# Kernel tuning notes

Measured on AMD Instinct MI355X. Metric: run time of the kernel, lower is better.

The kernel has to match this reference:

```python
import jax, jax.numpy as jnp
import numpy as np
import math

B, SQ, SK = 8, 1024, 1024
DIM_Q = DIM_K = DIM_V = 512
H = 8
EPS = 1e-5
INF = jnp.float32(1e38)


def _ln(x, g, b):
    mu = jnp.mean(x, axis=-1, keepdims=True)
    var = jnp.mean(jnp.square(x - mu), axis=-1, keepdims=True)
    return (x - mu) * jax.lax.rsqrt(var + EPS) * g + b


def setup_inputs() -> dict:
    key = jax.random.key(0)
    ks = jax.random.split(key, 12)
    s = 1.0 / math.sqrt(DIM_V)
    return {
        "queries": jax.random.normal(ks[0], (B, SQ, DIM_Q), jnp.float32),
        "keys": jax.random.normal(ks[1], (B, SK, DIM_K), jnp.float32),
        # binary presence masks (as in the original usage)
        "presence_q": (jax.random.uniform(ks[2], (B, SQ)) > 0.1).astype(jnp.float32),
        "presence_k": (jax.random.uniform(ks[3], (B, SK)) > 0.1).astype(jnp.float32),
        "num_heads": H,
        "Wq": jax.random.normal(ks[4], (DIM_Q, DIM_V), jnp.float32) * s,
        "bq": jnp.zeros((DIM_V,), jnp.float32),
        "Wk": jax.random.normal(ks[5], (DIM_K, DIM_V), jnp.float32) * s,
        "bk": jnp.zeros((DIM_V,), jnp.float32),
        "Wv": jax.random.normal(ks[6], (DIM_K, DIM_V), jnp.float32) * s,
        "bv": jnp.zeros((DIM_V,), jnp.float32),
        "Wo": jax.random.normal(ks[7], (DIM_V, DIM_V), jnp.float32) * s,
        "bo": jnp.zeros((DIM_V,), jnp.float32),
        "g0": jnp.ones((DIM_V,), jnp.float32),
        "b0": jnp.zeros((DIM_V,), jnp.float32),
        "g1": jnp.ones((DIM_V,), jnp.float32),
        "b1": jnp.zeros((DIM_V,), jnp.float32),
    }


def reference(queries, keys, presence_q, presence_k, num_heads,
              Wq, bq, Wk, bk, Wv, bv, Wo, bo, g0, b0, g1, b1):
    b, sq, _ = queries.shape
    dim_v = Wq.shape[1]
    d = dim_v // num_heads
    q = queries @ Wq + bq                              # [B,Sq,V]
    k = keys @ Wk + bk                                 # [B,Sk,V]
    v = keys @ Wv + bv                                 # [B,Sk,V]
    qh = q.reshape(b, sq, num_heads, d)
    kh = k.reshape(b, -1, num_heads, d)
    vh = v.reshape(b, -1, num_heads, d)
    logits = jnp.einsum('bqhd,bkhd->bhqk', qh, kh) / jnp.float32(math.sqrt(dim_v))
    pq = presence_q[:, None, :, None]                  # [B,1,Sq,1]
    logits = pq * logits - (1.0 - pq) * INF
    pk = presence_k[:, None, None, :]                  # [B,1,1,Sk]
    logits = pk * logits - (1.0 - pk) * INF
    A = jax.nn.softmax(logits, axis=-1)                # [B,H,Sq,Sk]
    o = qh + jnp.einsum('bhqk,bkhd->bqhd', A, vh)      # residual add of Q_
    o = o.reshape(b, sq, dim_v)
    o = _ln(o, g0, b0)
    o = o + jax.nn.relu(o @ Wo + bo)
    o = _ln(o, g1, b1)
    return o
```

## Files before the change

### kernel.cpp

```cpp
#include <hip/hip_runtime.h>

typedef __attribute__((ext_vector_type(8))) short short8;
typedef __attribute__((ext_vector_type(4))) float f32x4;

#define SCALE2 0.06375871571f

__device__ __forceinline__ float bfu(unsigned short u){
  return __uint_as_float(((unsigned int)u) << 16);
}
__device__ __forceinline__ unsigned short f2b(float x){
  unsigned int b = __float_as_uint(x);
  return (unsigned short)((b + 0x7fffu + ((b>>16)&1u)) >> 16);
}
__device__ __forceinline__ uint4 pack8(const float* f){
  float4 a = *(const float4*)f, b = *(const float4*)(f+4);
  uint4 r;
  r.x = (unsigned)f2b(a.x) | ((unsigned)f2b(a.y)<<16);
  r.y = (unsigned)f2b(a.z) | ((unsigned)f2b(a.w)<<16);
  r.z = (unsigned)f2b(b.x) | ((unsigned)f2b(b.y)<<16);
  r.w = (unsigned)f2b(b.z) | ((unsigned)f2b(b.w)<<16);
  return r;
}

__global__ __launch_bounds__(256) void prep_inputs(
    const float* Wq, const float* Wk, const float* Wv, const float* Wo,
    const float* q, const float* k, unsigned short* wt, unsigned short* qk_dst)
{
  const int id = blockIdx.x, t = threadIdx.x;
  if (id < 256){
    const int m = id >> 6;
    const float* W = (m==0)?Wq:(m==1)?Wk:(m==2)?Wv:Wo;
    unsigned short* dst = wt + (long)m*262144;
    __shared__ unsigned short tile[64][72];
    const int n0 = ((id>>3)&7)*64, k0 = (id&7)*64;
    {
      int r = t>>2, c0 = (t&3)*16;
      uint4 u0 = pack8(W + (long)(k0+r)*512 + n0 + c0);
      uint4 u1 = pack8(W + (long)(k0+r)*512 + n0 + c0 + 8);
      unsigned short* us0 = (unsigned short*)&u0;
      unsigned short* us1 = (unsigned short*)&u1;
      #pragma unroll
      for (int i=0;i<8;++i) tile[c0+i][r] = us0[i];
      #pragma unroll
      for (int i=0;i<8;++i) tile[c0+8+i][r] = us1[i];
    }
    __syncthreads();
    {
      int n = t>>2, ks = (t&3)*16;
      *(uint4*)(dst + (long)(n0+n)*512 + k0 + ks)     = *(uint4*)&tile[n][ks];
      *(uint4*)(dst + (long)(n0+n)*512 + k0 + ks + 8) = *(uint4*)&tile[n][ks+8];
    }
  } else {
    long i = ((long)(id-256)*256 + t)*8;
    const float* src = (i < 4194304) ? q + i : k + (i - 4194304);
    *(uint4*)(qk_dst + i) = pack8(src);
  }
}

__global__ __launch_bounds__(256) void proj_mfma(
    const unsigned short* qin, const unsigned short* kin, const unsigned short* wt,
    const float* bq, const float* bk, const float* bv,
    unsigned short* q_bf, unsigned short* k_bf, unsigned short* vt_bf)
{
  const int mat = blockIdx.z;
  const unsigned short* A = (mat==0)? qin : kin;
  const unsigned short* Wt = wt + (long)mat*262144;
  const float* bias = (mat==0)?bq:(mat==1)?bk:bv;
  const int row0 = blockIdx.y*128, col0 = blockIdx.x*128;
  __shared__ unsigned short As[2][128][40];
  __shared__ unsigned short Ws[2][128][40];
  const int t = threadIdx.x;
  const int lane = t & 63, wid = t >> 6;
  const int ln = lane & 15, quad = lane >> 4;
  const int wy = wid >> 1, wx = wid & 1;
  f32x4 acc[4][4];
  #pragma unroll
  for (int i=0;i<4;++i){
    #pragma unroll
    for (int j=0;j<4;++j) acc[i][j] = (f32x4){0.f,0.f,0.f,0.f};
  }
  const int sr = t>>1, sk0 = (t&1)*16;
  const unsigned short* Arow = A  + (long)(row0+sr)*512 + sk0;
  const unsigned short* Wrow = Wt + (long)(col0+sr)*512 + sk0;
  uint4 a0 = *(const uint4*)(Arow);
  uint4 a1 = *(const uint4*)(Arow + 8);
  uint4 w0 = *(const uint4*)(Wrow);
  uint4 w1 = *(const uint4*)(Wrow + 8);
  *(uint4*)&As[0][sr][sk0]   = a0;
  *(uint4*)&As[0][sr][sk0+8] = a1;
  *(uint4*)&Ws[0][sr][sk0]   = w0;
  *(uint4*)&Ws[0][sr][sk0+8] = w1;
  __syncthreads();
  for (int it=0; it<16; ++it){
    const int cur = it & 1;
    if (it < 15){
      a0 = *(const uint4*)(Arow + (it+1)*32);
      a1 = *(const uint4*)(Arow + (it+1)*32 + 8);
      w0 = *(const uint4*)(Wrow + (it+1)*32);
      w1 = *(const uint4*)(Wrow + (it+1)*32 + 8);
    }
    short8 a[4], b[4];
    #pragma unroll
    for (int mt=0;mt<4;++mt) a[mt] = *(const short8*)&As[cur][wy*64+mt*16+ln][quad*8];
    #pragma unroll
    for (int nt=0;nt<4;++nt) b[nt] = *(const short8*)&Ws[cur][wx*64+nt*16+ln][quad*8];
    #pragma unroll
    for (int mt=0;mt<4;++mt){
      #pragma unroll
      for (int nt=0;nt<4;++nt)
        acc[mt][nt] = __builtin_amdgcn_mfma_f32_16x16x32_bf16(a[mt], b[nt], acc[mt][nt], 0,0,0);
    }
    if (it < 15){
      *(uint4*)&As[cur^1][sr][sk0]   = a0;
      *(uint4*)&As[cur^1][sr][sk0+8] = a1;
      *(uint4*)&Ws[cur^1][sr][sk0]   = w0;
      *(uint4*)&Ws[cur^1][sr][sk0+8] = w1;
    }
    __syncthreads();
  }
  float bias_v[4];
  #pragma unroll
  for (int nt=0;nt<4;++nt) bias_v[nt] = bias[col0 + wx*64 + nt*16 + ln];
  if (mat < 2){
    unsigned short* dst = (mat==0)? q_bf : k_bf;
    #pragma unroll
    for (int mt=0;mt<4;++mt){
      int row = row0 + wy*64 + mt*16 + quad*4;
      #pragma unroll
      for (int nt=0;nt<4;++nt){
        int col = col0 + wx*64 + nt*16 + ln;
        #pragma unroll
        for (int r=0;r<4;++r)
          dst[(long)(row+r)*512 + col] = f2b(acc[mt][nt][r] + bias_v[nt]);
      }
    }
  } else {
    #pragma unroll
    for (int mt=0;mt<4;++mt){
      int row = row0 + wy*64 + mt*16 + quad*4;
      int bb = row >> 10, sk = row & 1023;
      #pragma unroll
      for (int nt=0;nt<4;++nt){
        int col = col0 + wx*64 + nt*16 + ln;
        int h = col >> 6, dd = col & 63;
        uint2 pk2; unsigned short* pp = (unsigned short*)&pk2;
        #pragma unroll
        for (int r=0;r<4;++r) pp[r] = f2b(acc[mt][nt][r] + bias_v[nt]);
        *(uint2*)(vt_bf + (((long)((bb*8+h)*64+dd)) << 10) + sk) = pk2;
      }
    }
  }
}

__global__ __launch_bounds__(512) void attn_mfma(
    const unsigned short* q_bf, const unsigned short* k_bf, const unsigned short* vt_bf,
    const float* pres_q, const float* pres_k, unsigned short* o_bf)
{
  const int bx = blockIdx.x;
  const int b = bx >> 3, h = bx & 7;
  const int q0 = blockIdx.y * 128;
  const int t = threadIdx.x;
  const int lane = t & 63, wid = t >> 6, ln = lane & 15, quad = lane >> 4;
  __shared__ unsigned short QP[128][72];
  __shared__ unsigned short Ks[2][64][72];
  __shared__ unsigned short Vt[2][64][72];
  __shared__ float pq_s[128];
  __shared__ float pk_s[2][64];
  {
    int tok = t>>2, ds = (t&3)*16;
    const unsigned short* src = q_bf + (long)(b*1024 + q0 + tok)*512 + h*64 + ds;
    *(uint4*)&QP[tok][ds]   = *(const uint4*)src;
    *(uint4*)&QP[tok][ds+8] = *(const uint4*)(src+8);
  }
  {
    int tok = t>>3, ds = (t&7)*8;
    *(uint4*)&Ks[0][tok][ds] = *(const uint4*)(k_bf + (long)(b*1024 + tok)*512 + h*64 + ds);
    *(uint4*)&Vt[0][tok][ds] = *(const uint4*)(vt_bf + (((long)((b*8+h)*64 + tok)) << 10) + ds);
  }
  if (t < 128) pq_s[t] = pres_q[b*1024 + q0 + t];
  if (t < 64)  pk_s[0][t] = pres_k[b*1024 + t];
  __syncthreads();
  short8 aq0 = *(const short8*)&QP[wid*16+ln][quad*8];
  short8 aq1 = *(const short8*)&QP[wid*16+ln][32+quad*8];
  float av[4], mval[4];
  #pragma unroll
  for (int r=0;r<4;++r){
    av[r] = pq_s[wid*16 + quad*4 + r]*SCALE2;
    mval[r] = (av[r] == 0.f) ? 0.f : -43.f;
  }
  f32x4 oacc[4];
  #pragma unroll
  for (int dt=0;dt<4;++dt) oacc[dt] = (f32x4){0.f,0.f,0.f,0.f};
  float lsum[4] = {0.f,0.f,0.f,0.f};

  for (int it=0; it<16; ++it){
    const int cur = it & 1;
    const int k0n = (it+1)*64;
    uint4 pf_k, pf_v; float pf_p = 0.f;
    if (it < 15){
      int tok = t>>3, ds = (t&7)*8;
      pf_k = *(const uint4*)(k_bf + (long)(b*1024 + k0n + tok)*512 + h*64 + ds);
      pf_v = *(const uint4*)(vt_bf + (((long)((b*8+h)*64 + tok)) << 10) + k0n + ds);
      if (t < 64) pf_p = pres_k[b*1024 + k0n + t];
    }
    f32x4 s[4];
    #pragma unroll
    for (int kt=0;kt<4;++kt) s[kt] = (f32x4){0.f,0.f,0.f,0.f};
    #pragma unroll
    for (int kt=0;kt<4;++kt){
      short8 kb0 = *(const short8*)&Ks[cur][kt*16+ln][quad*8];
      short8 kb1 = *(const short8*)&Ks[cur][kt*16+ln][32+quad*8];
      s[kt] = __builtin_amdgcn_mfma_f32_16x16x32_bf16(aq0, kb0, s[kt], 0,0,0);
      s[kt] = __builtin_amdgcn_mfma_f32_16x16x32_bf16(aq1, kb1, s[kt], 0,0,0);
    }
    float pk4[4];
    #pragma unroll
    for (int kt=0;kt<4;++kt) pk4[kt] = pk_s[cur][kt*16+ln];
    #pragma unroll
    for (int r=0;r<4;++r){
      #pragma unroll
      for (int kt=0;kt<4;++kt){
        float x0 = s[kt][r]*av[r];
        float x = __builtin_fmaf(pk4[kt], x0 - mval[r], mval[r]);
        float e = __builtin_amdgcn_exp2f(x);
        lsum[r] += e;
        QP[wid*16+quad*4+r][kt*16+ln] = (unsigned short)(__float_as_uint(e) >> 16);
      }
    }
    short8 ap0 = *(const short8*)&QP[wid*16+ln][quad*8];
    short8 ap1 = *(const short8*)&QP[wid*16+ln][32+quad*8];
    #pragma unroll
    for (int dt=0;dt<4;++dt){
      short8 vb0 = *(const short8*)&Vt[cur][dt*16+ln][quad*8];
      short8 vb1 = *(const short8*)&Vt[cur][dt*16+ln][32+quad*8];
      oacc[dt] = __builtin_amdgcn_mfma_f32_16x16x32_bf16(ap0, vb0, oacc[dt], 0,0,0);
      oacc[dt] = __builtin_amdgcn_mfma_f32_16x16x32_bf16(ap1, vb1, oacc[dt], 0,0,0);
    }
    if (it < 15){
      int tok = t>>3, ds = (t&7)*8;
      *(uint4*)&Ks[cur^1][tok][ds] = pf_k;
      *(uint4*)&Vt[cur^1][tok][ds] = pf_v;
      if (t < 64) pk_s[cur^1][t] = pf_p;
    }
    __syncthreads();
  }
  #pragma unroll
  for (int r=0;r<4;++r){
    float l = lsum[r];
    #pragma unroll
    for (int msk=1; msk<16; msk<<=1) l += __shfl_xor(l, msk);
    float inv = 1.f / l;
    int ql = wid*16 + quad*4 + r;
    long base = (long)(b*1024 + q0 + ql)*512 + h*64;
    #pragma unroll
    for (int dt=0;dt<4;++dt){
      float qh = bfu(q_bf[base + dt*16 + ln]);
      o_bf[base + dt*16 + ln] = f2b(qh + oacc[dt][r]*inv);
    }
  }
}

__global__ __launch_bounds__(256) void ln_kernel(
    const unsigned short* in, void* outp, int mode, const float* g, const float* bvec)
{
  const int row = blockIdx.x*4 + (threadIdx.x >> 6);
  const int lane = threadIdx.x & 63;
  uint4 raw = *(const uint4*)(in + (long)row*512 + lane*8);
  const unsigned short* rs16 = (const unsigned short*)&raw;
  float v[8];
  #pragma unroll
  for (int c=0;c<8;++c) v[c] = bfu(rs16[c]);
  float sum = 0.f;
  #pragma unroll
  for (int c=0;c<8;++c) sum += v[c];
  #pragma unroll
  for (int msk=1; msk<64; msk<<=1) sum += __shfl_xor(sum, msk);
  float mu = sum * (1.f/512.f);
  float var = 0.f;
  #pragma unroll
  for (int c=0;c<8;++c){ v[c] -= mu; var += v[c]*v[c]; }
  #pragma unroll
  for (int msk=1; msk<64; msk<<=1) var += __shfl_xor(var, msk);
  float rs = rsqrtf(var*(1.f/512.f) + 1e-5f);
  float gv[8], bv[8];
  *(float4*)&gv[0] = *(const float4*)(g + lane*8);
  *(float4*)&gv[4] = *(const float4*)(g + lane*8 + 4);
  *(float4*)&bv[0] = *(const float4*)(bvec + lane*8);
  *(float4*)&bv[4] = *(const float4*)(bvec + lane*8 + 4);
  float y[8];
  #pragma unroll
  for (int c=0;c<8;++c) y[c] = v[c]*rs*gv[c] + bv[c];
  if (mode){
    float* dst = (float*)outp + (long)row*512 + lane*8;
    *(float4*)dst       = *(float4*)&y[0];
    *(float4*)(dst + 4) = *(float4*)&y[4];
  } else {
    uint4 out; unsigned short* os = (unsigned short*)&out;
    #pragma unroll
    for (int c=0;c<8;++c) os[c] = f2b(y[c]);
    *(uint4*)((unsigned short*)outp + (long)row*512 + lane*8) = out;
  }
}

__global__ __launch_bounds__(256) void out_mfma(
    const unsigned short* t_bf, const unsigned short* Wt, const float* bo,
    unsigned short* u_bf)
{
  const int row0 = blockIdx.y*64, col0 = blockIdx.x*128;
  __shared__ unsigned short As[2][64][40];
  __shared__ unsigned short Ws[2][128][40];
  const int t = threadIdx.x;
  const int lane = t & 63, wid = t >> 6;
  const int ln = lane & 15, quad = lane >> 4;
  const int wy = wid >> 1, wx = wid & 1;
  f32x4 acc[2][4];
  #pragma unroll
  for (int i=0;i<2;++i){
    #pragma unroll
    for (int j=0;j<4;++j) acc[i][j] = (f32x4){0.f,0.f,0.f,0.f};
  }
  const int ar = t>>2, ac0 = (t&3)*8;
  const int wr = t>>1, wc0 = (t&1)*16;
  const unsigned short* Arow = t_bf + (long)(row0+ar)*512 + ac0;
  const unsigned short* Wrow = Wt   + (long)(col0+wr)*512 + wc0;
  uint4 a0 = *(const uint4*)(Arow);
  uint4 w0 = *(const uint4*)(Wrow);
  uint4 w1 = *(const uint4*)(Wrow + 8);
  *(uint4*)&As[0][ar][ac0] = a0;
  *(uint4*)&Ws[0][wr][wc0]   = w0;
  *(uint4*)&Ws[0][wr][wc0+8] = w1;
  __syncthreads();
  for (int it=0; it<16; ++it){
    const int cur = it & 1;
    if (it < 15){
      a0 = *(const uint4*)(Arow + (it+1)*32);
      w0 = *(const uint4*)(Wrow + (it+1)*32);
      w1 = *(const uint4*)(Wrow + (it+1)*32 + 8);
    }
    short8 a[2], b[4];
    #pragma unroll
    for (int mt=0;mt<2;++mt) a[mt] = *(const short8*)&As[cur][wy*32+mt*16+ln][quad*8];
    #pragma unroll
    for (int nt=0;nt<4;++nt) b[nt] = *(const short8*)&Ws[cur][wx*64+nt*16+ln][quad*8];
    #pragma unroll
    for (int mt=0;mt<2;++mt){
      #pragma unroll
      for (int nt=0;nt<4;++nt)
        acc[mt][nt] = __builtin_amdgcn_mfma_f32_16x16x32_bf16(a[mt], b[nt], acc[mt][nt], 0,0,0);
    }
    if (it < 15){
      *(uint4*)&As[cur^1][ar][ac0] = a0;
      *(uint4*)&Ws[cur^1][wr][wc0]   = w0;
      *(uint4*)&Ws[cur^1][wr][wc0+8] = w1;
    }
    __syncthreads();
  }
  float bias_v[4];
  #pragma unroll
  for (int nt=0;nt<4;++nt) bias_v[nt] = bo[col0 + wx*64 + nt*16 + ln];
  #pragma unroll
  for (int mt=0;mt<2;++mt){
    int row = row0 + wy*32 + mt*16 + quad*4;
    #pragma unroll
    for (int nt=0;nt<4;++nt){
      int col = col0 + wx*64 + nt*16 + ln;
      #pragma unroll
      for (int r=0;r<4;++r){
        long idx = (long)(row+r)*512 + col;
        float u = acc[mt][nt][r] + bias_v[nt];
        u = fmaxf(u, 0.f);
        u_bf[idx] = f2b(bfu(t_bf[idx]) + u);
      }
    }
  }
}

extern "C" void kernel_launch(void* const* d_in, const int* in_sizes, int n_in,
                              void* d_out, int out_size, void* d_ws, size_t ws_size,
                              hipStream_t stream)
{
  unsigned short* q_bf  = (unsigned short*)d_ws;
  unsigned short* k_bf  = q_bf  + 8192l*512;
  unsigned short* vt_bf = k_bf  + 8192l*512;
  unsigned short* t_bf  = vt_bf + 8192l*512;
  unsigned short* wt    = t_bf  + 8192l*512;
  unsigned short* qin   = wt + 4l*512*512;
  unsigned short* kin   = qin + 4194304;
  unsigned short* o_bf  = qin;
  unsigned short* u_bf  = kin;

  hipLaunchKernelGGL(prep_inputs, dim3(4352), dim3(256), 0, stream,
                     (const float*)d_in[5], (const float*)d_in[7],
                     (const float*)d_in[9], (const float*)d_in[11],
                     (const float*)d_in[0], (const float*)d_in[1], wt, qin);
  hipLaunchKernelGGL(proj_mfma, dim3(4,64,3), dim3(256), 0, stream,
                     qin, kin, wt,
                     (const float*)d_in[6], (const float*)d_in[8],
                     (const float*)d_in[10], q_bf, k_bf, vt_bf);
  hipLaunchKernelGGL(attn_mfma, dim3(64,8), dim3(512), 0, stream,
                     q_bf, k_bf, vt_bf,
                     (const float*)d_in[2], (const float*)d_in[3], o_bf);
  hipLaunchKernelGGL(ln_kernel, dim3(2048), dim3(256), 0, stream,
                     o_bf, (void*)t_bf, 0, (const float*)d_in[13], (const float*)d_in[14]);
  hipLaunchKernelGGL(out_mfma, dim3(4,128), dim3(256), 0, stream,
                     t_bf, wt + 3l*512*512, (const float*)d_in[12], u_bf);
  hipLaunchKernelGGL(ln_kernel, dim3(2048), dim3(256), 0, stream,
                     u_bf, d_out, 1, (const float*)d_in[15], (const float*)d_in[16]);
}
```

Before: 208.3 us.

## Halve attention block to 4 waves, each handling 32 query rows

The attention kernel now runs 256 threads (4 waves) per 128-query block instead of 8 waves. Each wave processes two 16-row query subtiles, so every K and V fragment read from LDS feeds two MFMAs. The cooperative loads and prefetches are widened so the 4 waves still fill the tiles. This cuts LDS traffic per MFMA and barrier participants, but raises register use and leaves fewer waves to hide latency.

```diff
diff --git a/kernel.cpp b/kernel.cpp
--- a/kernel.cpp
+++ b/kernel.cpp
@@ -152,7 +152,7 @@
   }
 }
 
-__global__ __launch_bounds__(512) void attn_mfma(
+__global__ __launch_bounds__(256) void attn_mfma(
     const unsigned short* q_bf, const unsigned short* k_bf, const unsigned short* vt_bf,
     const float* pres_q, const float* pres_k, unsigned short* o_bf)
 {
@@ -167,95 +167,133 @@
   __shared__ float pq_s[128];
   __shared__ float pk_s[2][64];
   {
+    int tok = t>>1, ds = (t&1)*32;
+    const unsigned short* src = q_bf + (long)(b*1024 + q0 + tok)*512 + h*64 + ds;
+    *(uint4*)&QP[tok][ds]    = *(const uint4*)src;
+    *(uint4*)&QP[tok][ds+8]  = *(const uint4*)(src+8);
+    *(uint4*)&QP[tok][ds+16] = *(const uint4*)(src+16);
+    *(uint4*)&QP[tok][ds+24] = *(const uint4*)(src+24);
+  }
+  {
     int tok = t>>2, ds = (t&3)*16;
-    const unsigned short* src = q_bf + (long)(b*1024 + q0 + tok)*512 + h*64 + ds;
-    *(uint4*)&QP[tok][ds]   = *(const uint4*)src;
-    *(uint4*)&QP[tok][ds+8] = *(const uint4*)(src+8);
-  }
-  {
-    int tok = t>>3, ds = (t&7)*8;
-    *(uint4*)&Ks[0][tok][ds] = *(const uint4*)(k_bf + (long)(b*1024 + tok)*512 + h*64 + ds);
-    *(uint4*)&Vt[0][tok][ds] = *(const uint4*)(vt_bf + (((long)((b*8+h)*64 + tok)) << 10) + ds);
+    const unsigned short* sk = k_bf + (long)(b*1024 + tok)*512 + h*64 + ds;
+    *(uint4*)&Ks[0][tok][ds]   = *(const uint4*)sk;
+    *(uint4*)&Ks[0][tok][ds+8] = *(const uint4*)(sk+8);
+    const unsigned short* sv = vt_bf + (((long)((b*8+h)*64 + tok)) << 10) + ds;
+    *(uint4*)&Vt[0][tok][ds]   = *(const uint4*)sv;
+    *(uint4*)&Vt[0][tok][ds+8] = *(const uint4*)(sv+8);
   }
   if (t < 128) pq_s[t] = pres_q[b*1024 + q0 + t];
   if (t < 64)  pk_s[0][t] = pres_k[b*1024 + t];
   __syncthreads();
-  short8 aq0 = *(const short8*)&QP[wid*16+ln][quad*8];
-  short8 aq1 = *(const short8*)&QP[wid*16+ln][32+quad*8];
-  float av[4], mval[4];
-  #pragma unroll
-  for (int r=0;r<4;++r){
-    av[r] = pq_s[wid*16 + quad*4 + r]*SCALE2;
-    mval[r] = (av[r] == 0.f) ? 0.f : -43.f;
-  }
-  f32x4 oacc[4];
-  #pragma unroll
-  for (int dt=0;dt<4;++dt) oacc[dt] = (f32x4){0.f,0.f,0.f,0.f};
-  float lsum[4] = {0.f,0.f,0.f,0.f};
+  short8 aq[2][2];
+  float av[2][4], mval[2][4];
+  #pragma unroll
+  for (int s=0;s<2;++s){
+    aq[s][0] = *(const short8*)&QP[wid*32+s*16+ln][quad*8];
+    aq[s][1] = *(const short8*)&QP[wid*32+s*16+ln][32+quad*8];
+    #pragma unroll
+    for (int r=0;r<4;++r){
+      av[s][r] = pq_s[wid*32 + s*16 + quad*4 + r]*SCALE2;
+      mval[s][r] = (av[s][r] == 0.f) ? 0.f : -43.f;
+    }
+  }
+  f32x4 oacc[2][4];
+  float lsum[2][4];
+  #pragma unroll
+  for (int s=0;s<2;++s){
+    #pragma unroll
+    for (int i=0;i<4;++i){ oacc[s][i] = (f32x4){0.f,0.f,0.f,0.f}; lsum[s][i] = 0.f; }
+  }
 
   for (int it=0; it<16; ++it){
     const int cur = it & 1;
     const int k0n = (it+1)*64;
-    uint4 pf_k, pf_v; float pf_p = 0.f;
-    if (it < 15){
-      int tok = t>>3, ds = (t&7)*8;
-      pf_k = *(const uint4*)(k_bf + (long)(b*1024 + k0n + tok)*512 + h*64 + ds);
-      pf_v = *(const uint4*)(vt_bf + (((long)((b*8+h)*64 + tok)) << 10) + k0n + ds);
+    uint4 pf_k0, pf_k1, pf_v0, pf_v1; float pf_p = 0.f;
+    if (it < 15){
+      int tok = t>>2, ds = (t&3)*16;
+      const unsigned short* sk = k_bf + (long)(b*1024 + k0n + tok)*512 + h*64 + ds;
+      pf_k0 = *(const uint4*)sk;
+      pf_k1 = *(const uint4*)(sk+8);
+      const unsigned short* sv = vt_bf + (((long)((b*8+h)*64 + tok)) << 10) + k0n + ds;
+      pf_v0 = *(const uint4*)sv;
+      pf_v1 = *(const uint4*)(sv+8);
       if (t < 64) pf_p = pres_k[b*1024 + k0n + t];
     }
-    f32x4 s[4];
-    #pragma unroll
-    for (int kt=0;kt<4;++kt) s[kt] = (f32x4){0.f,0.f,0.f,0.f};
+    f32x4 s[2][4];
+    #pragma unroll
+    for (int st=0;st<2;++st){
+      #pragma unroll
+      for (int kt=0;kt<4;++kt) s[st][kt] = (f32x4){0.f,0.f,0.f,0.f};
+    }
     #pragma unroll
     for (int kt=0;kt<4;++kt){
       short8 kb0 = *(const short8*)&Ks[cur][kt*16+ln][quad*8];
       short8 kb1 = *(const short8*)&Ks[cur][kt*16+ln][32+quad*8];
-      s[kt] = __builtin_amdgcn_mfma_f32_16x16x32_bf16(aq0, kb0, s[kt], 0,0,0);
-      s[kt] = __builtin_amdgcn_mfma_f32_16x16x32_bf16(aq1, kb1, s[kt], 0,0,0);
+      #pragma unroll
+      for (int st=0;st<2;++st){
+        s[st][kt] = __builtin_amdgcn_mfma_f32_16x16x32_bf16(aq[st][0], kb0, s[st][kt], 0,0,0);
+        s[st][kt] = __builtin_amdgcn_mfma_f32_16x16x32_bf16(aq[st][1], kb1, s[st][kt], 0,0,0);
+      }
     }
     float pk4[4];
     #pragma unroll
     for (int kt=0;kt<4;++kt) pk4[kt] = pk_s[cur][kt*16+ln];
     #pragma unroll
-    for (int r=0;r<4;++r){
-      #pragma unroll
-      for (int kt=0;kt<4;++kt){
-        float x0 = s[kt][r]*av[r];
-        float x = __builtin_fmaf(pk4[kt], x0 - mval[r], mval[r]);
-        float e = __builtin_amdgcn_exp2f(x);
-        lsum[r] += e;
-        QP[wid*16+quad*4+r][kt*16+ln] = (unsigned short)(__float_as_uint(e) >> 16);
-      }
-    }
-    short8 ap0 = *(const short8*)&QP[wid*16+ln][quad*8];
-    short8 ap1 = *(const short8*)&QP[wid*16+ln][32+quad*8];
+    for (int st=0;st<2;++st){
+      #pragma unroll
+      for (int r=0;r<4;++r){
+        #pragma unroll
+        for (int kt=0;kt<4;++kt){
+          float x0 = s[st][kt][r]*av[st][r];
+          float x = __builtin_fmaf(pk4[kt], x0 - mval[st][r], mval[st][r]);
+          float e = __builtin_amdgcn_exp2f(x);
+          lsum[st][r] += e;
+          QP[wid*32+st*16+quad*4+r][kt*16+ln] = (unsigned short)(__float_as_uint(e) >> 16);
+        }
+      }
+    }
+    short8 ap[2][2];
+    #pragma unroll
+    for (int st=0;st<2;++st){
+      ap[st][0] = *(const short8*)&QP[wid*32+st*16+ln][quad*8];
+      ap[st][1] = *(const short8*)&QP[wid*32+st*16+ln][32+quad*8];
+    }
     #pragma unroll
     for (int dt=0;dt<4;++dt){
       short8 vb0 = *(const short8*)&Vt[cur][dt*16+ln][quad*8];
       short8 vb1 = *(const short8*)&Vt[cur][dt*16+ln][32+quad*8];
-      oacc[dt] = __builtin_amdgcn_mfma_f32_16x16x32_bf16(ap0, vb0, oacc[dt], 0,0,0);
-      oacc[dt] = __builtin_amdgcn_mfma_f32_16x16x32_bf16(ap1, vb1, oacc[dt], 0,0,0);
-    }
-    if (it < 15){
-      int tok = t>>3, ds = (t&7)*8;
-      *(uint4*)&Ks[cur^1][tok][ds] = pf_k;
-      *(uint4*)&Vt[cur^1][tok][ds] = pf_v;
+      #pragma unroll
+      for (int st=0;st<2;++st){
+        oacc[st][dt] = __builtin_amdgcn_mfma_f32_16x16x32_bf16(ap[st][0], vb0, oacc[st][dt], 0,0,0);
+        oacc[st][dt] = __builtin_amdgcn_mfma_f32_16x16x32_bf16(ap[st][1], vb1, oacc[st][dt], 0,0,0);
+      }
+    }
+    if (it < 15){
+      int tok = t>>2, ds = (t&3)*16;
+      *(uint4*)&Ks[cur^1][tok][ds]   = pf_k0;
+      *(uint4*)&Ks[cur^1][tok][ds+8] = pf_k1;
+      *(uint4*)&Vt[cur^1][tok][ds]   = pf_v0;
+      *(uint4*)&Vt[cur^1][tok][ds+8] = pf_v1;
       if (t < 64) pk_s[cur^1][t] = pf_p;
     }
     __syncthreads();
   }
   #pragma unroll
-  for (int r=0;r<4;++r){
-    float l = lsum[r];
-    #pragma unroll
-    for (int msk=1; msk<16; msk<<=1) l += __shfl_xor(l, msk);
-    float inv = 1.f / l;
-    int ql = wid*16 + quad*4 + r;
-    long base = (long)(b*1024 + q0 + ql)*512 + h*64;
-    #pragma unroll
-    for (int dt=0;dt<4;++dt){
-      float qh = bfu(q_bf[base + dt*16 + ln]);
-      o_bf[base + dt*16 + ln] = f2b(qh + oacc[dt][r]*inv);
+  for (int st=0;st<2;++st){
+    #pragma unroll
+    for (int r=0;r<4;++r){
+      float l = lsum[st][r];
+      #pragma unroll
+      for (int msk=1; msk<16; msk<<=1) l += __shfl_xor(l, msk);
+      float inv = 1.f / l;
+      int ql = wid*32 + st*16 + quad*4 + r;
+      long base = (long)(b*1024 + q0 + ql)*512 + h*64;
+      #pragma unroll
+      for (int dt=0;dt<4;++dt){
+        float qh = bfu(q_bf[base + dt*16 + ln]);
+        o_bf[base + dt*16 + ln] = f2b(qh + oacc[st][dt][r]*inv);
+      }
     }
   }
 }
@@ -397,7 +435,7 @@
                      qin, kin, wt,
                      (const float*)d_in[6], (const float*)d_in[8],
                      (const float*)d_in[10], q_bf, k_bf, vt_bf);
-  hipLaunchKernelGGL(attn_mfma, dim3(64,8), dim3(512), 0, stream,
+  hipLaunchKernelGGL(attn_mfma, dim3(64,8), dim3(256), 0, stream,
                      q_bf, k_bf, vt_bf,
                      (const float*)d_in[2], (const float*)d_in[3], o_bf);
   hipLaunchKernelGGL(ln_kernel, dim3(2048), dim3(256), 0, stream,
```

Result: no change. 207.2 us (-0.5%).
